# Kernel tuning notes

Measured on AMD Instinct MI355X. Metric: run time of the kernel, lower is better.

Reference implementation:

```python
import jax, jax.numpy as jnp
import numpy as np

C = 256


def _conv1x1(x, w, b):
    # x: [B,C,H,W], w: [O,C], b: [O] -> 1x1 conv == per-pixel linear
    return jnp.einsum('bchw,oc->bohw', x, w) + b[None, :, None, None]


def setup_inputs() -> dict:
    key = jax.random.key(0)
    ks = jax.random.split(key, 10)
    B, H, W = 4, 64, 64
    scale = 1.0 / np.sqrt(C)
    inp = {
        'F_c': jax.random.normal(ks[0], (B, C, H, W), jnp.float32),
        'F_s': jax.random.normal(ks[1], (B, C, H, W), jnp.float32),
        'w_f': jax.random.normal(ks[2], (C, C), jnp.float32) * scale,
        'b_f': jax.random.normal(ks[3], (C,), jnp.float32) * 0.01,
        'w_g': jax.random.normal(ks[4], (C, C), jnp.float32) * scale,
        'b_g': jax.random.normal(ks[5], (C,), jnp.float32) * 0.01,
        'w_h': jax.random.normal(ks[6], (C, C), jnp.float32) * scale,
        'b_h': jax.random.normal(ks[7], (C,), jnp.float32) * 0.01,
        'w_o': jax.random.normal(ks[8], (C, C), jnp.float32) * scale,
        'b_o': jax.random.normal(ks[9], (C,), jnp.float32) * 0.01,
    }
    return inp


def reference(F_c, F_s, w_f, b_f, w_g, b_g, w_h, b_h, w_o, b_o):
    b, c, h, w = F_c.shape
    Fq = _conv1x1(F_c, w_f, b_f).reshape(b, c, -1)   # [B,C,Nq]
    G = _conv1x1(F_s, w_g, b_g).reshape(b, c, -1)    # [B,C,Nk]
    Hv = _conv1x1(F_s, w_h, b_h).reshape(b, c, -1)   # [B,C,Nk]
    # S[b,i,j] = sum_c Fq[b,c,i] * G[b,c,j]; softmax over keys j
    S = jax.nn.softmax(jnp.einsum('bci,bcj->bij', Fq, G), axis=-1)
    # result[b,c,i] = sum_j Hv[b,c,j] * S[b,i,j]
    res = jnp.einsum('bcj,bij->bci', Hv, S).reshape(b, c, h, w)
    return _conv1x1(res, w_o, b_o)
```

## Files before the change

kernel.cpp:

```cpp
#include <hip/hip_runtime.h>
#include <hip/hip_bf16.h>

typedef __attribute__((ext_vector_type(8))) short bf16x8;
typedef __attribute__((ext_vector_type(4))) float f32x4;
typedef __attribute__((ext_vector_type(8))) _Float16 f16x8;
typedef __attribute__((ext_vector_type(8))) unsigned short u16x8;
typedef __attribute__((ext_vector_type(4))) unsigned short u16x4;
typedef unsigned int uint32;
typedef unsigned short ushort;

#define MFMA16(a, b, c) __builtin_amdgcn_mfma_f32_16x16x32_bf16((a), (b), (c), 0, 0, 0)
#define MFMA16F(a, b, c) __builtin_amdgcn_mfma_f32_16x16x32_f16((a), (b), (c), 0, 0, 0)

__device__ __forceinline__ ushort f2bf(float f) {
    __hip_bfloat16 h = __float2bfloat16(f);
    return __builtin_bit_cast(ushort, h);
}
__device__ __forceinline__ float bf2f(ushort u) {
    uint32 v = ((uint32)u) << 16;
    return __builtin_bit_cast(float, v);
}
__device__ __forceinline__ void gld16(const ushort* g, ushort* l) {
    __builtin_amdgcn_global_load_lds(
        (const __attribute__((address_space(1))) unsigned int*)g,
        (__attribute__((address_space(3))) unsigned int*)l, 16, 0, 0);
}

__global__ __launch_bounds__(256) void transpose_split(
    const float* __restrict__ Fc, const float* __restrict__ Fs,
    ushort* __restrict__ XcH, ushort* __restrict__ XcL,
    ushort* __restrict__ XsH, ushort* __restrict__ XsL) {
    __shared__ float lds[64][65];
    const int z = blockIdx.z;
    const int b = z & 3;
    const float* src = (z < 4) ? Fc : Fs;
    ushort* dh = (z < 4) ? XcH : XsH;
    ushort* dl = (z < 4) ? XcL : XsL;
    src += (size_t)b * 256 * 4096;
    dh += (size_t)b * 4096 * 256;
    dl += (size_t)b * 4096 * 256;
    const int i0 = blockIdx.x * 64;
    const int c0 = blockIdx.y * 64;
    const int t = threadIdx.x;
    const int rq = t >> 4;
    const int q4 = (t & 15) * 4;
#pragma unroll
    for (int p = 0; p < 4; p++) {
        int r = rq + p * 16;
        float4 v = *(const float4*)(src + (size_t)(c0 + r) * 4096 + i0 + q4);
        lds[q4 + 0][r] = v.x;
        lds[q4 + 1][r] = v.y;
        lds[q4 + 2][r] = v.z;
        lds[q4 + 3][r] = v.w;
    }
    __syncthreads();
#pragma unroll
    for (int p = 0; p < 4; p++) {
        int i = rq + p * 16;
        u16x4 hv, lv;
#pragma unroll
        for (int e = 0; e < 4; e++) {
            float f = lds[i][q4 + e];
            ushort hb = f2bf(f);
            hv[e] = hb;
            lv[e] = f2bf(f - bf2f(hb));
        }
        *(u16x4*)(dh + (size_t)(i0 + i) * 256 + c0 + q4) = hv;
        *(u16x4*)(dl + (size_t)(i0 + i) * 256 + c0 + q4) = lv;
    }
}

__global__ __launch_bounds__(256) void convert_weights(
    const float* __restrict__ wf, const float* __restrict__ wg,
    const float* __restrict__ wh, const float* __restrict__ wo,
    ushort* __restrict__ wfh, ushort* __restrict__ wfl,
    ushort* __restrict__ wgh, ushort* __restrict__ wgl,
    ushort* __restrict__ whb, ushort* __restrict__ wob) {
    const int t = blockIdx.x * 256 + threadIdx.x;
    const float L2E = 1.4426950408889634f;
    float sf = wf[t] * L2E;
    ushort hf = f2bf(sf);
    wfh[t] = hf;
    wfl[t] = f2bf(sf - bf2f(hf));
    float sg = wg[t];
    ushort hg = f2bf(sg);
    wgh[t] = hg;
    wgl[t] = f2bf(sg - bf2f(hg));
    whb[t] = f2bf(wh[t]);
    wob[t] = f2bf(wo[t]);
}

__global__ __launch_bounds__(256) void proj_qk(
    const ushort* __restrict__ XcH, const ushort* __restrict__ XcL,
    const ushort* __restrict__ XsH, const ushort* __restrict__ XsL,
    const ushort* __restrict__ wfh, const ushort* __restrict__ wfl,
    const ushort* __restrict__ wgh, const ushort* __restrict__ wgl,
    const float* __restrict__ bf_, const float* __restrict__ bg_,
    _Float16* __restrict__ QF, _Float16* __restrict__ KF) {
    const int y = blockIdx.y;
    const int isK = y >> 2;
    const int b = y & 3;
    const size_t bNC = (size_t)b * 4096 * 256;
    const ushort* Ah = (isK ? XsH : XcH) + bNC;
    const ushort* Al = (isK ? XsL : XcL) + bNC;
    const ushort* Bh = isK ? wgh : wfh;
    const ushort* Bl = isK ? wgl : wfl;
    const float* bias = isK ? bg_ : bf_;
    const float bscale = isK ? 1.0f : 1.4426950408889634f;
    _Float16* Co = (isK ? KF : QF) + bNC;
    const int m0 = (blockIdx.x & 63) * 64, n0 = (blockIdx.x >> 6) * 64;
    const int l = threadIdx.x & 63, wv = threadIdx.x >> 6;
    const int g = l >> 4, l15 = l & 15;
    const int mrow = m0 + wv * 16 + l15;

    f32x4 acc[4] = {{0, 0, 0, 0}, {0, 0, 0, 0}, {0, 0, 0, 0}, {0, 0, 0, 0}};
#pragma unroll
    for (int kk = 0; kk < 8; kk++) {
        bf16x8 ah = *(const bf16x8*)(Ah + (size_t)mrow * 256 + kk * 32 + g * 8);
        bf16x8 al = *(const bf16x8*)(Al + (size_t)mrow * 256 + kk * 32 + g * 8);
#pragma unroll
        for (int nt = 0; nt < 4; nt++) {
            const size_t boff = (size_t)(n0 + nt * 16 + l15) * 256 + kk * 32 + g * 8;
            bf16x8 bh = *(const bf16x8*)(Bh + boff);
            bf16x8 bl = *(const bf16x8*)(Bl + boff);
            acc[nt] = MFMA16(ah, bh, acc[nt]);
            acc[nt] = MFMA16(ah, bl, acc[nt]);
            acc[nt] = MFMA16(al, bh, acc[nt]);
        }
    }
#pragma unroll
    for (int nt = 0; nt < 4; nt++) {
        float bn = bias[n0 + nt * 16 + l15] * bscale;
#pragma unroll
        for (int r = 0; r < 4; r++) {
            int mr = m0 + wv * 16 + g * 4 + r;
            Co[(size_t)mr * 256 + n0 + nt * 16 + l15] = (_Float16)(acc[nt][r] + bn);
        }
    }
}

__global__ __launch_bounds__(256) void proj_v(
    const ushort* __restrict__ XsH, const ushort* __restrict__ whb,
    const float* __restrict__ bh_, ushort* __restrict__ Vv) {
    const int b = blockIdx.y;
    const size_t bNC = (size_t)b * 4096 * 256;
    const ushort* A = whb;
    const ushort* Bp = XsH + bNC;
    ushort* Cp = Vv + bNC;
    const int m0 = (blockIdx.x & 3) * 64, n0 = (blockIdx.x >> 2) * 64;
    const int l = threadIdx.x & 63, wv = threadIdx.x >> 6;
    const int g = l >> 4, l15 = l & 15;
    const int mrow = m0 + wv * 16 + l15;

    f32x4 acc[4] = {{0, 0, 0, 0}, {0, 0, 0, 0}, {0, 0, 0, 0}, {0, 0, 0, 0}};
#pragma unroll
    for (int kk = 0; kk < 8; kk++) {
        bf16x8 af = *(const bf16x8*)(A + (size_t)mrow * 256 + kk * 32 + g * 8);
#pragma unroll
        for (int nt = 0; nt < 4; nt++) {
            bf16x8 bfr = *(const bf16x8*)(Bp + (size_t)(n0 + nt * 16 + l15) * 256 + kk * 32 + g * 8);
            acc[nt] = MFMA16(af, bfr, acc[nt]);
        }
    }
#pragma unroll
    for (int nt = 0; nt < 4; nt++) {
#pragma unroll
        for (int r = 0; r < 4; r++) {
            int mr = m0 + wv * 16 + g * 4 + r;
            Cp[(size_t)mr * 4096 + n0 + nt * 16 + l15] = f2bf(acc[nt][r] + bh_[mr]);
        }
    }
}

__global__ __launch_bounds__(512, 2) void attn_split(
    const _Float16* __restrict__ QF, const _Float16* __restrict__ KF,
    const ushort* __restrict__ Vv, _Float16* __restrict__ Opart,
    float2* __restrict__ ML) {
    __shared__ __align__(16) _Float16 Kf[2][32 * 256];
    __shared__ __align__(16) ushort Vt[2][256 * 40];

    const int h = blockIdx.x;
    const int grp = h & 7;
    const int itile = h >> 3;
    const int b = grp >> 1;
    const int s = grp & 1;

    const int tid = threadIdx.x;
    const int l = tid & 63, wv = tid >> 6;
    const int g = l >> 4, l15 = l & 15;
    const int iw = itile * 128 + wv * 16;
    const _Float16* Qb = QF + ((size_t)b * 4096 + iw) * 256;
    const _Float16* Kb = KF + (size_t)b * 4096 * 256;
    const ushort* Vb = Vv + (size_t)b * 4096 * 256;

    f16x8 qf[8];
#pragma unroll
    for (int kk = 0; kk < 8; kk++)
        qf[kk] = *(const f16x8*)(Qb + (size_t)l15 * 256 + kk * 32 + g * 8);

    const int vch = tid >> 1;
    const int vko = (tid & 1) * 16;
    const ushort* Vsrc = Vb + (size_t)vch * 4096;

    f32x4 acc[16];
#pragma unroll
    for (int ct = 0; ct < 16; ct++) acc[ct] = (f32x4){0, 0, 0, 0};
    float M = -INFINITY, Lsum = 0.0f;

    const int jbeg = s * 2048, jend = jbeg + 2048;

    auto stageK = [&](int buf, int jj) {
        const _Float16* ks = Kb + (size_t)jj * 256;
#pragma unroll
        for (int q = 0; q < 2; q++) {
            int issue = wv * 2 + q;
            int row = issue * 2 + (l >> 5);
            int scol = ((l & 31) ^ row) * 8;
            gld16((const ushort*)(ks + (size_t)row * 256 + scol),
                  (ushort*)&Kf[buf][issue * 512]);
        }
    };

    stageK(0, jbeg);
    {
        u16x8 va = *(const u16x8*)(Vsrc + jbeg + vko);
        u16x8 vb2 = *(const u16x8*)(Vsrc + jbeg + vko + 8);
        asm volatile("s_waitcnt vmcnt(0)" ::: "memory");
        *(u16x8*)&Vt[0][vch * 40 + vko] = va;
        *(u16x8*)&Vt[0][vch * 40 + vko + 8] = vb2;
    }
    __syncthreads();

    int cur = 0;
    for (int j0 = jbeg; j0 < jend; j0 += 32) {
        const bool pre = (j0 + 32) < jend;
        u16x8 va, vb2;
        if (pre) {
            stageK(cur ^ 1, j0 + 32);
            va = *(const u16x8*)(Vsrc + (j0 + 32) + vko);
            vb2 = *(const u16x8*)(Vsrc + (j0 + 32) + vko + 8);
        }
        f32x4 s0e = {0, 0, 0, 0}, s0o = {0, 0, 0, 0};
        f32x4 s1e = {0, 0, 0, 0}, s1o = {0, 0, 0, 0};
        const int r1 = l15 + 16;
#pragma unroll
        for (int kk = 0; kk < 8; kk += 2) {
            {
                int cs = kk * 4 + g;
                f16x8 k0 = *(const f16x8*)&Kf[cur][l15 * 256 + ((cs ^ l15) & 31) * 8];
                f16x8 k1 = *(const f16x8*)&Kf[cur][r1 * 256 + ((cs ^ r1) & 31) * 8];
                s0e = MFMA16F(k0, qf[kk], s0e);
                s1e = MFMA16F(k1, qf[kk], s1e);
            }
            {
                int cs = (kk + 1) * 4 + g;
                f16x8 k0 = *(const f16x8*)&Kf[cur][l15 * 256 + ((cs ^ l15) & 31) * 8];
                f16x8 k1 = *(const f16x8*)&Kf[cur][r1 * 256 + ((cs ^ r1) & 31) * 8];
                s0o = MFMA16F(k0, qf[kk + 1], s0o);
                s1o = MFMA16F(k1, qf[kk + 1], s1o);
            }
        }
        f32x4 s0 = s0e + s0o;
        f32x4 s1 = s1e + s1o;
        float tm = fmaxf(fmaxf(fmaxf(s0[0], s0[1]), fmaxf(s0[2], s0[3])),
                         fmaxf(fmaxf(s1[0], s1[1]), fmaxf(s1[2], s1[3])));
        tm = fmaxf(tm, __shfl_xor(tm, 16));
        tm = fmaxf(tm, __shfl_xor(tm, 32));
        if (__any(tm - M > 8.0f)) {
            float newM = fmaxf(M, tm);
            float alpha = exp2f(M - newM);
            Lsum *= alpha;
            float ar[4];
#pragma unroll
            for (int r = 0; r < 4; r++) ar[r] = __shfl(alpha, g * 4 + r);
#pragma unroll
            for (int ct = 0; ct < 16; ct++) {
#pragma unroll
                for (int r = 0; r < 4; r++) acc[ct][r] *= ar[r];
            }
            M = newM;
        }
        float p[8];
#pragma unroll
        for (int r = 0; r < 4; r++) {
            p[r] = exp2f(s0[r] - M);
            p[4 + r] = exp2f(s1[r] - M);
        }
        Lsum += p[0] + p[1] + p[2] + p[3] + p[4] + p[5] + p[6] + p[7];

        uint32 pk[4];
        pk[0] = (uint32)f2bf(p[0]) | ((uint32)f2bf(p[1]) << 16);
        pk[1] = (uint32)f2bf(p[2]) | ((uint32)f2bf(p[3]) << 16);
        pk[2] = (uint32)f2bf(p[4]) | ((uint32)f2bf(p[5]) << 16);
        pk[3] = (uint32)f2bf(p[6]) | ((uint32)f2bf(p[7]) << 16);
        const int ts = g >> 1;
        const int s1l = l15 + ((g & 1) << 5);
        uint32 w0a = __shfl(pk[0], s1l), w0b = __shfl(pk[2], s1l);
        uint32 w1a = __shfl(pk[1], s1l), w1b = __shfl(pk[3], s1l);
        uint32 w2a = __shfl(pk[0], s1l + 16), w2b = __shfl(pk[2], s1l + 16);
        uint32 w3a = __shfl(pk[1], s1l + 16), w3b = __shfl(pk[3], s1l + 16);
        union { uint32 u[4]; bf16x8 v; } pun;
        pun.u[0] = ts ? w0b : w0a;
        pun.u[1] = ts ? w1b : w1a;
        pun.u[2] = ts ? w2b : w2a;
        pun.u[3] = ts ? w3b : w3a;
        bf16x8 pf = pun.v;

#pragma unroll
        for (int ct = 0; ct < 16; ct++) {
            bf16x8 vf = *(const bf16x8*)&Vt[cur][(ct * 16 + l15) * 40 + g * 8];
            acc[ct] = MFMA16(pf, vf, acc[ct]);
        }
        if (pre) {
            asm volatile("s_waitcnt vmcnt(0)" ::: "memory");
            *(u16x8*)&Vt[cur ^ 1][vch * 40 + vko] = va;
            *(u16x8*)&Vt[cur ^ 1][vch * 40 + vko + 8] = vb2;
        }
        __syncthreads();
        cur ^= 1;
    }
    float Lt = Lsum + __shfl_xor(Lsum, 16);
    Lt += __shfl_xor(Lt, 32);
    float inv = 1.0f / Lt;
    float ivr[4];
#pragma unroll
    for (int r = 0; r < 4; r++) ivr[r] = __shfl(inv, g * 4 + r);
    const size_t sb = (size_t)(s * 4 + b);
    _Float16* Ob = Opart + (sb * 4096 + iw) * 256;
#pragma unroll
    for (int ct = 0; ct < 16; ct++) {
#pragma unroll
        for (int r = 0; r < 4; r++)
            Ob[(size_t)(g * 4 + r) * 256 + ct * 16 + l15] =
                (_Float16)(acc[ct][r] * ivr[r]);
    }
    if (g == 0) {
        float2 ml;
        ml.x = M;
        ml.y = Lt;
        ML[sb * 4096 + iw + l15] = ml;
    }
}

__global__ __launch_bounds__(256) void attn_combine(
    const _Float16* __restrict__ Opart, const float2* __restrict__ ML,
    ushort* __restrict__ Rt) {
    const int b = blockIdx.y;
    const int i = blockIdx.x * 8 + (threadIdx.x >> 5);
    const int c0 = (threadIdx.x & 31) * 8;
    float2 ml0 = ML[(size_t)(0 * 4 + b) * 4096 + i];
    float2 ml1 = ML[(size_t)(1 * 4 + b) * 4096 + i];
    float Mmax = fmaxf(ml0.x, ml1.x);
    float w0 = ml0.y * exp2f(ml0.x - Mmax);
    float w1 = ml1.y * exp2f(ml1.x - Mmax);
    float inv = 1.0f / (w0 + w1);
    w0 *= inv;
    w1 *= inv;
    f16x8 v0 = *(const f16x8*)(Opart + ((size_t)(0 * 4 + b) * 4096 + i) * 256 + c0);
    f16x8 v1 = *(const f16x8*)(Opart + ((size_t)(1 * 4 + b) * 4096 + i) * 256 + c0);
    u16x8 r;
#pragma unroll
    for (int e = 0; e < 8; e++) r[e] = f2bf(w0 * (float)v0[e] + w1 * (float)v1[e]);
    *(u16x8*)(Rt + ((size_t)b * 4096 + i) * 256 + c0) = r;
}

__global__ __launch_bounds__(256) void out_proj(
    const ushort* __restrict__ wob, const ushort* __restrict__ Rt,
    const float* __restrict__ bo, float* __restrict__ Out) {
    const int b = blockIdx.y;
    const int m0 = (blockIdx.x & 3) * 64;
    const int n0 = (blockIdx.x >> 2) * 64;
    const int l = threadIdx.x & 63, wv = threadIdx.x >> 6;
    const int g = l >> 4, l15 = l & 15;
    const ushort* Bp = Rt + (size_t)b * 4096 * 256;
    float* Ob = Out + (size_t)b * 256 * 4096;
    const int mrow = m0 + wv * 16 + l15;

    f32x4 acc[4] = {{0, 0, 0, 0}, {0, 0, 0, 0}, {0, 0, 0, 0}, {0, 0, 0, 0}};
#pragma unroll
    for (int kk = 0; kk < 8; kk++) {
        bf16x8 af = *(const bf16x8*)(wob + (size_t)mrow * 256 + kk * 32 + g * 8);
#pragma unroll
        for (int nt = 0; nt < 4; nt++) {
            bf16x8 bfr = *(const bf16x8*)(Bp + (size_t)(n0 + nt * 16 + l15) * 256 + kk * 32 + g * 8);
            acc[nt] = MFMA16(af, bfr, acc[nt]);
        }
    }
#pragma unroll
    for (int nt = 0; nt < 4; nt++) {
#pragma unroll
        for (int r = 0; r < 4; r++) {
            int mr = m0 + wv * 16 + g * 4 + r;
            Ob[(size_t)mr * 4096 + n0 + nt * 16 + l15] = acc[nt][r] + bo[mr];
        }
    }
}

extern "C" void kernel_launch(void* const* d_in, const int* in_sizes, int n_in,
                              void* d_out, int out_size, void* d_ws, size_t ws_size,
                              hipStream_t stream) {
    const float* Fc = (const float*)d_in[0];
    const float* Fs = (const float*)d_in[1];
    const float* wf = (const float*)d_in[2];
    const float* bf_ = (const float*)d_in[3];
    const float* wg = (const float*)d_in[4];
    const float* bg = (const float*)d_in[5];
    const float* wh = (const float*)d_in[6];
    const float* bh = (const float*)d_in[7];
    const float* wo = (const float*)d_in[8];
    const float* bo = (const float*)d_in[9];
    float* Out = (float*)d_out;

    char* ws = (char*)d_ws;
    const size_t SZ = (size_t)4 * 4096 * 256 * 2;
    _Float16* QFp = (_Float16*)(ws + 0 * SZ);
    _Float16* KFp = (_Float16*)(ws + 1 * SZ);
    ushort* Vv  = (ushort*)(ws + 2 * SZ);
    ushort* XcH = (ushort*)(ws + 3 * SZ);
    ushort* XcL = (ushort*)(ws + 4 * SZ);
    ushort* XsH = (ushort*)(ws + 5 * SZ);
    ushort* XsL = (ushort*)(ws + 6 * SZ);
    _Float16* Opart = (_Float16*)(ws + 3 * SZ);
    char* wsw = ws + 7 * SZ;
    ushort* wfh = (ushort*)(wsw + 0 * 131072);
    ushort* wfl = (ushort*)(wsw + 1 * 131072);
    ushort* wgh = (ushort*)(wsw + 2 * 131072);
    ushort* wgl = (ushort*)(wsw + 3 * 131072);
    ushort* whb = (ushort*)(wsw + 4 * 131072);
    ushort* wob = (ushort*)(wsw + 5 * 131072);
    float2* ML = (float2*)(wsw + 6 * 131072);
    ushort* Rt = (ushort*)QFp;

    transpose_split<<<dim3(64, 4, 8), 256, 0, stream>>>(Fc, Fs, XcH, XcL, XsH, XsL);
    convert_weights<<<dim3(256), 256, 0, stream>>>(wf, wg, wh, wo, wfh, wfl, wgh, wgl, whb, wob);
    proj_qk<<<dim3(256, 8), 256, 0, stream>>>(XcH, XcL, XsH, XsL, wfh, wfl, wgh, wgl,
                                              bf_, bg, QFp, KFp);
    proj_v<<<dim3(256, 4), 256, 0, stream>>>(XsH, whb, bh, Vv);
    attn_split<<<dim3(256), 512, 0, stream>>>(QFp, KFp, Vv, Opart, ML);
    attn_combine<<<dim3(512, 4), 256, 0, stream>>>(Opart, ML, Rt);
    out_proj<<<dim3(256, 4), 256, 0, stream>>>(wob, Rt, bo, Out);
}
```

Before: 352.9 us.

## Switch pipeline to fp16, use 32x32 MFMA attention with 4-way key split

Activations are now converted to a single fp16 copy instead of bf16 hi/lo pairs. This halves transpose output traffic and drops one of the three MFMAs in the Q/K projection. The attention kernel moves to 32x32x16 f16 MFMA with 32 query rows per wave, uses v_permlane32_swap to repack P, and splits keys four ways instead of two, so the combine kernel now merges four partials. The intent is less memory traffic and better MFMA efficiency. The risks are fp16 range and precision limits on activations, plus extra partial-output traffic.

```diff
diff --git a/kernel.cpp b/kernel.cpp
--- a/kernel.cpp
+++ b/kernel.cpp
@@ -1,44 +1,37 @@
 #include <hip/hip_runtime.h>
 #include <hip/hip_bf16.h>
 
-typedef __attribute__((ext_vector_type(8))) short bf16x8;
 typedef __attribute__((ext_vector_type(4))) float f32x4;
+typedef __attribute__((ext_vector_type(16))) float f32x16;
 typedef __attribute__((ext_vector_type(8))) _Float16 f16x8;
-typedef __attribute__((ext_vector_type(8))) unsigned short u16x8;
-typedef __attribute__((ext_vector_type(4))) unsigned short u16x4;
+typedef __attribute__((ext_vector_type(4))) _Float16 f16x4;
 typedef unsigned int uint32;
 typedef unsigned short ushort;
 
-#define MFMA16(a, b, c) __builtin_amdgcn_mfma_f32_16x16x32_bf16((a), (b), (c), 0, 0, 0)
 #define MFMA16F(a, b, c) __builtin_amdgcn_mfma_f32_16x16x32_f16((a), (b), (c), 0, 0, 0)
-
-__device__ __forceinline__ ushort f2bf(float f) {
-    __hip_bfloat16 h = __float2bfloat16(f);
-    return __builtin_bit_cast(ushort, h);
-}
-__device__ __forceinline__ float bf2f(ushort u) {
-    uint32 v = ((uint32)u) << 16;
-    return __builtin_bit_cast(float, v);
-}
-__device__ __forceinline__ void gld16(const ushort* g, ushort* l) {
+#define MFMA32F(a, b, c) __builtin_amdgcn_mfma_f32_32x32x16_f16((a), (b), (c), 0, 0, 0)
+
+__device__ __forceinline__ uint32 pkf16(float a, float b) {
+    ushort ua = __builtin_bit_cast(ushort, (_Float16)a);
+    ushort ub = __builtin_bit_cast(ushort, (_Float16)b);
+    return (uint32)ua | ((uint32)ub << 16);
+}
+__device__ __forceinline__ void gld16(const _Float16* g, _Float16* l) {
     __builtin_amdgcn_global_load_lds(
         (const __attribute__((address_space(1))) unsigned int*)g,
         (__attribute__((address_space(3))) unsigned int*)l, 16, 0, 0);
 }
 
-__global__ __launch_bounds__(256) void transpose_split(
+__global__ __launch_bounds__(256) void transpose_f16(
     const float* __restrict__ Fc, const float* __restrict__ Fs,
-    ushort* __restrict__ XcH, ushort* __restrict__ XcL,
-    ushort* __restrict__ XsH, ushort* __restrict__ XsL) {
+    _Float16* __restrict__ Xc, _Float16* __restrict__ Xs) {
     __shared__ float lds[64][65];
     const int z = blockIdx.z;
     const int b = z & 3;
     const float* src = (z < 4) ? Fc : Fs;
-    ushort* dh = (z < 4) ? XcH : XsH;
-    ushort* dl = (z < 4) ? XcL : XsL;
+    _Float16* dst = (z < 4) ? Xc : Xs;
     src += (size_t)b * 256 * 4096;
-    dh += (size_t)b * 4096 * 256;
-    dl += (size_t)b * 4096 * 256;
+    dst += (size_t)b * 4096 * 256;
     const int i0 = blockIdx.x * 64;
     const int c0 = blockIdx.y * 64;
     const int t = threadIdx.x;
@@ -57,54 +50,46 @@
 #pragma unroll
     for (int p = 0; p < 4; p++) {
         int i = rq + p * 16;
-        u16x4 hv, lv;
-#pragma unroll
-        for (int e = 0; e < 4; e++) {
-            float f = lds[i][q4 + e];
-            ushort hb = f2bf(f);
-            hv[e] = hb;
-            lv[e] = f2bf(f - bf2f(hb));
-        }
-        *(u16x4*)(dh + (size_t)(i0 + i) * 256 + c0 + q4) = hv;
-        *(u16x4*)(dl + (size_t)(i0 + i) * 256 + c0 + q4) = lv;
+        f16x4 hv;
+#pragma unroll
+        for (int e = 0; e < 4; e++) hv[e] = (_Float16)lds[i][q4 + e];
+        *(f16x4*)(dst + (size_t)(i0 + i) * 256 + c0 + q4) = hv;
     }
 }
 
 __global__ __launch_bounds__(256) void convert_weights(
     const float* __restrict__ wf, const float* __restrict__ wg,
     const float* __restrict__ wh, const float* __restrict__ wo,
-    ushort* __restrict__ wfh, ushort* __restrict__ wfl,
-    ushort* __restrict__ wgh, ushort* __restrict__ wgl,
-    ushort* __restrict__ whb, ushort* __restrict__ wob) {
+    _Float16* __restrict__ wfh, _Float16* __restrict__ wfl,
+    _Float16* __restrict__ wgh, _Float16* __restrict__ wgl,
+    _Float16* __restrict__ whb, _Float16* __restrict__ wob) {
     const int t = blockIdx.x * 256 + threadIdx.x;
     const float L2E = 1.4426950408889634f;
     float sf = wf[t] * L2E;
-    ushort hf = f2bf(sf);
+    _Float16 hf = (_Float16)sf;
     wfh[t] = hf;
-    wfl[t] = f2bf(sf - bf2f(hf));
+    wfl[t] = (_Float16)(sf - (float)hf);
     float sg = wg[t];
-    ushort hg = f2bf(sg);
+    _Float16 hg = (_Float16)sg;
     wgh[t] = hg;
-    wgl[t] = f2bf(sg - bf2f(hg));
-    whb[t] = f2bf(wh[t]);
-    wob[t] = f2bf(wo[t]);
+    wgl[t] = (_Float16)(sg - (float)hg);
+    whb[t] = (_Float16)wh[t];
+    wob[t] = (_Float16)wo[t];
 }
 
 __global__ __launch_bounds__(256) void proj_qk(
-    const ushort* __restrict__ XcH, const ushort* __restrict__ XcL,
-    const ushort* __restrict__ XsH, const ushort* __restrict__ XsL,
-    const ushort* __restrict__ wfh, const ushort* __restrict__ wfl,
-    const ushort* __restrict__ wgh, const ushort* __restrict__ wgl,
+    const _Float16* __restrict__ Xc, const _Float16* __restrict__ Xs,
+    const _Float16* __restrict__ wfh, const _Float16* __restrict__ wfl,
+    const _Float16* __restrict__ wgh, const _Float16* __restrict__ wgl,
     const float* __restrict__ bf_, const float* __restrict__ bg_,
     _Float16* __restrict__ QF, _Float16* __restrict__ KF) {
     const int y = blockIdx.y;
     const int isK = y >> 2;
     const int b = y & 3;
     const size_t bNC = (size_t)b * 4096 * 256;
-    const ushort* Ah = (isK ? XsH : XcH) + bNC;
-    const ushort* Al = (isK ? XsL : XcL) + bNC;
-    const ushort* Bh = isK ? wgh : wfh;
-    const ushort* Bl = isK ? wgl : wfl;
+    const _Float16* A = (isK ? Xs : Xc) + bNC;
+    const _Float16* Bh = isK ? wgh : wfh;
+    const _Float16* Bl = isK ? wgl : wfl;
     const float* bias = isK ? bg_ : bf_;
     const float bscale = isK ? 1.0f : 1.4426950408889634f;
     _Float16* Co = (isK ? KF : QF) + bNC;
@@ -116,16 +101,14 @@
     f32x4 acc[4] = {{0, 0, 0, 0}, {0, 0, 0, 0}, {0, 0, 0, 0}, {0, 0, 0, 0}};
 #pragma unroll
     for (int kk = 0; kk < 8; kk++) {
-        bf16x8 ah = *(const bf16x8*)(Ah + (size_t)mrow * 256 + kk * 32 + g * 8);
-        bf16x8 al = *(const bf16x8*)(Al + (size_t)mrow * 256 + kk * 32 + g * 8);
+        f16x8 a = *(const f16x8*)(A + (size_t)mrow * 256 + kk * 32 + g * 8);
 #pragma unroll
         for (int nt = 0; nt < 4; nt++) {
             const size_t boff = (size_t)(n0 + nt * 16 + l15) * 256 + kk * 32 + g * 8;
-            bf16x8 bh = *(const bf16x8*)(Bh + boff);
-            bf16x8 bl = *(const bf16x8*)(Bl + boff);
-            acc[nt] = MFMA16(ah, bh, acc[nt]);
-            acc[nt] = MFMA16(ah, bl, acc[nt]);
-            acc[nt] = MFMA16(al, bh, acc[nt]);
+            f16x8 bh = *(const f16x8*)(Bh + boff);
+            f16x8 bl = *(const f16x8*)(Bl + boff);
+            acc[nt] = MFMA16F(a, bh, acc[nt]);
+            acc[nt] = MFMA16F(a, bl, acc[nt]);
         }
     }
 #pragma unroll
@@ -140,13 +123,12 @@
 }
 
 __global__ __launch_bounds__(256) void proj_v(
-    const ushort* __restrict__ XsH, const ushort* __restrict__ whb,
-    const float* __restrict__ bh_, ushort* __restrict__ Vv) {
+    const _Float16* __restrict__ Xs, const _Float16* __restrict__ whb,
+    const float* __restrict__ bh_, _Float16* __restrict__ VF) {
     const int b = blockIdx.y;
     const size_t bNC = (size_t)b * 4096 * 256;
-    const ushort* A = whb;
-    const ushort* Bp = XsH + bNC;
-    ushort* Cp = Vv + bNC;
+    const _Float16* Bp = Xs + bNC;
+    _Float16* Cp = VF + bNC;
     const int m0 = (blockIdx.x & 3) * 64, n0 = (blockIdx.x >> 2) * 64;
     const int l = threadIdx.x & 63, wv = threadIdx.x >> 6;
     const int g = l >> 4, l15 = l & 15;
@@ -155,11 +137,11 @@
     f32x4 acc[4] = {{0, 0, 0, 0}, {0, 0, 0, 0}, {0, 0, 0, 0}, {0, 0, 0, 0}};
 #pragma unroll
     for (int kk = 0; kk < 8; kk++) {
-        bf16x8 af = *(const bf16x8*)(A + (size_t)mrow * 256 + kk * 32 + g * 8);
+        f16x8 a = *(const f16x8*)(whb + (size_t)mrow * 256 + kk * 32 + g * 8);
 #pragma unroll
         for (int nt = 0; nt < 4; nt++) {
-            bf16x8 bfr = *(const bf16x8*)(Bp + (size_t)(n0 + nt * 16 + l15) * 256 + kk * 32 + g * 8);
-            acc[nt] = MFMA16(af, bfr, acc[nt]);
+            f16x8 bfr = *(const f16x8*)(Bp + (size_t)(n0 + nt * 16 + l15) * 256 + kk * 32 + g * 8);
+            acc[nt] = MFMA16F(a, bfr, acc[nt]);
         }
     }
 #pragma unroll
@@ -167,47 +149,47 @@
 #pragma unroll
         for (int r = 0; r < 4; r++) {
             int mr = m0 + wv * 16 + g * 4 + r;
-            Cp[(size_t)mr * 4096 + n0 + nt * 16 + l15] = f2bf(acc[nt][r] + bh_[mr]);
+            Cp[(size_t)mr * 4096 + n0 + nt * 16 + l15] = (_Float16)(acc[nt][r] + bh_[mr]);
         }
     }
 }
 
 __global__ __launch_bounds__(512, 2) void attn_split(
     const _Float16* __restrict__ QF, const _Float16* __restrict__ KF,
-    const ushort* __restrict__ Vv, _Float16* __restrict__ Opart,
+    const _Float16* __restrict__ VF, _Float16* __restrict__ Opart,
     float2* __restrict__ ML) {
-    __shared__ __align__(16) _Float16 Kf[2][32 * 256];
-    __shared__ __align__(16) ushort Vt[2][256 * 40];
+    __shared__ __align__(16) _Float16 Klds[2][32 * 256];
+    __shared__ __align__(16) _Float16 Vt[2][256 * 40];
 
     const int h = blockIdx.x;
-    const int grp = h & 7;
-    const int itile = h >> 3;
-    const int b = grp >> 1;
-    const int s = grp & 1;
+    const int grp = (h & 7) + 8 * ((h >> 3) & 1);
+    const int itile = h >> 4;
+    const int b = grp & 3, s = grp >> 2;
 
     const int tid = threadIdx.x;
     const int l = tid & 63, wv = tid >> 6;
-    const int g = l >> 4, l15 = l & 15;
-    const int iw = itile * 128 + wv * 16;
-    const _Float16* Qb = QF + ((size_t)b * 4096 + iw) * 256;
+    const int i31 = l & 31, hi = l >> 5;
+    const int iwq = itile * 256 + wv * 32;
+    const _Float16* Qb = QF + ((size_t)b * 4096 + iwq) * 256;
     const _Float16* Kb = KF + (size_t)b * 4096 * 256;
-    const ushort* Vb = Vv + (size_t)b * 4096 * 256;
-
-    f16x8 qf[8];
-#pragma unroll
-    for (int kk = 0; kk < 8; kk++)
-        qf[kk] = *(const f16x8*)(Qb + (size_t)l15 * 256 + kk * 32 + g * 8);
-
-    const int vch = tid >> 1;
-    const int vko = (tid & 1) * 16;
-    const ushort* Vsrc = Vb + (size_t)vch * 4096;
-
-    f32x4 acc[16];
-#pragma unroll
-    for (int ct = 0; ct < 16; ct++) acc[ct] = (f32x4){0, 0, 0, 0};
+    const _Float16* Vb = VF + (size_t)b * 4096 * 256;
+
+    f16x8 qf[16];
+#pragma unroll
+    for (int t = 0; t < 16; t++)
+        qf[t] = *(const f16x8*)(Qb + (size_t)i31 * 256 + t * 16 + hi * 8);
+
+    f32x16 acc[8];
+#pragma unroll
+    for (int ct = 0; ct < 8; ct++)
+#pragma unroll
+        for (int r = 0; r < 16; r++) acc[ct][r] = 0.0f;
     float M = -INFINITY, Lsum = 0.0f;
 
-    const int jbeg = s * 2048, jend = jbeg + 2048;
+    const int vch = tid >> 1, vko = (tid & 1) * 16;
+    const _Float16* Vsrc = Vb + (size_t)vch * 4096;
+
+    const int jbeg = s * 1024, jend = jbeg + 1024;
 
     auto stageK = [&](int buf, int jj) {
         const _Float16* ks = Kb + (size_t)jj * 256;
@@ -215,175 +197,174 @@
         for (int q = 0; q < 2; q++) {
             int issue = wv * 2 + q;
             int row = issue * 2 + (l >> 5);
-            int scol = ((l & 31) ^ row) * 8;
-            gld16((const ushort*)(ks + (size_t)row * 256 + scol),
-                  (ushort*)&Kf[buf][issue * 512]);
+            int scol = ((l & 31) ^ (row & 7)) * 8;
+            gld16(ks + (size_t)row * 256 + scol, &Klds[buf][issue * 512]);
         }
     };
 
     stageK(0, jbeg);
     {
-        u16x8 va = *(const u16x8*)(Vsrc + jbeg + vko);
-        u16x8 vb2 = *(const u16x8*)(Vsrc + jbeg + vko + 8);
+        f16x8 va = *(const f16x8*)(Vsrc + jbeg + vko);
+        f16x8 vb2 = *(const f16x8*)(Vsrc + jbeg + vko + 8);
         asm volatile("s_waitcnt vmcnt(0)" ::: "memory");
-        *(u16x8*)&Vt[0][vch * 40 + vko] = va;
-        *(u16x8*)&Vt[0][vch * 40 + vko + 8] = vb2;
+        *(f16x8*)&Vt[0][vch * 40 + vko] = va;
+        *(f16x8*)&Vt[0][vch * 40 + vko + 8] = vb2;
     }
     __syncthreads();
 
     int cur = 0;
     for (int j0 = jbeg; j0 < jend; j0 += 32) {
         const bool pre = (j0 + 32) < jend;
-        u16x8 va, vb2;
+        f16x8 va, vb2;
         if (pre) {
             stageK(cur ^ 1, j0 + 32);
-            va = *(const u16x8*)(Vsrc + (j0 + 32) + vko);
-            vb2 = *(const u16x8*)(Vsrc + (j0 + 32) + vko + 8);
-        }
-        f32x4 s0e = {0, 0, 0, 0}, s0o = {0, 0, 0, 0};
-        f32x4 s1e = {0, 0, 0, 0}, s1o = {0, 0, 0, 0};
-        const int r1 = l15 + 16;
-#pragma unroll
-        for (int kk = 0; kk < 8; kk += 2) {
-            {
-                int cs = kk * 4 + g;
-                f16x8 k0 = *(const f16x8*)&Kf[cur][l15 * 256 + ((cs ^ l15) & 31) * 8];
-                f16x8 k1 = *(const f16x8*)&Kf[cur][r1 * 256 + ((cs ^ r1) & 31) * 8];
-                s0e = MFMA16F(k0, qf[kk], s0e);
-                s1e = MFMA16F(k1, qf[kk], s1e);
-            }
-            {
-                int cs = (kk + 1) * 4 + g;
-                f16x8 k0 = *(const f16x8*)&Kf[cur][l15 * 256 + ((cs ^ l15) & 31) * 8];
-                f16x8 k1 = *(const f16x8*)&Kf[cur][r1 * 256 + ((cs ^ r1) & 31) * 8];
-                s0o = MFMA16F(k0, qf[kk + 1], s0o);
-                s1o = MFMA16F(k1, qf[kk + 1], s1o);
-            }
-        }
-        f32x4 s0 = s0e + s0o;
-        f32x4 s1 = s1e + s1o;
-        float tm = fmaxf(fmaxf(fmaxf(s0[0], s0[1]), fmaxf(s0[2], s0[3])),
-                         fmaxf(fmaxf(s1[0], s1[1]), fmaxf(s1[2], s1[3])));
-        tm = fmaxf(tm, __shfl_xor(tm, 16));
+            va = *(const f16x8*)(Vsrc + (j0 + 32) + vko);
+            vb2 = *(const f16x8*)(Vsrc + (j0 + 32) + vko + 8);
+        }
+        f32x16 sacc;
+#pragma unroll
+        for (int r = 0; r < 16; r++) sacc[r] = 0.0f;
+#pragma unroll
+        for (int t = 0; t < 16; t++) {
+            int pc = (2 * t + hi) ^ (i31 & 7);
+            f16x8 kf = *(const f16x8*)&Klds[cur][i31 * 256 + pc * 8];
+            sacc = MFMA32F(kf, qf[t], sacc);
+        }
+        float tm = sacc[0];
+#pragma unroll
+        for (int r = 1; r < 16; r++) tm = fmaxf(tm, sacc[r]);
         tm = fmaxf(tm, __shfl_xor(tm, 32));
         if (__any(tm - M > 8.0f)) {
             float newM = fmaxf(M, tm);
             float alpha = exp2f(M - newM);
             Lsum *= alpha;
-            float ar[4];
-#pragma unroll
-            for (int r = 0; r < 4; r++) ar[r] = __shfl(alpha, g * 4 + r);
-#pragma unroll
-            for (int ct = 0; ct < 16; ct++) {
-#pragma unroll
-                for (int r = 0; r < 4; r++) acc[ct][r] *= ar[r];
+            float ar[16];
+#pragma unroll
+            for (int r = 0; r < 16; r++)
+                ar[r] = __shfl(alpha, (r & 3) + 8 * (r >> 2) + 4 * hi);
+#pragma unroll
+            for (int ct = 0; ct < 8; ct++)
+#pragma unroll
+                for (int r = 0; r < 16; r++) acc[ct][r] *= ar[r];
+            M = newM;
+        }
+        float p[16], ps = 0.0f;
+#pragma unroll
+        for (int r = 0; r < 16; r++) {
+            p[r] = exp2f(sacc[r] - M);
+            ps += p[r];
+        }
+        Lsum += ps;
+        uint32 Pq[4][2];
+#pragma unroll
+        for (int q = 0; q < 4; q++) {
+            Pq[q][0] = pkf16(p[4 * q + 0], p[4 * q + 1]);
+            Pq[q][1] = pkf16(p[4 * q + 2], p[4 * q + 3]);
+        }
+#pragma unroll
+        for (int tp = 0; tp < 2; tp++) {
+            uint32 x0 = Pq[2 * tp][0], y0 = Pq[2 * tp + 1][0];
+            uint32 x1 = Pq[2 * tp][1], y1 = Pq[2 * tp + 1][1];
+            asm volatile("v_permlane32_swap_b32 %0, %1" : "+v"(x0), "+v"(y0));
+            asm volatile("v_permlane32_swap_b32 %0, %1" : "+v"(x1), "+v"(y1));
+            union { uint32 u[4]; f16x8 v; } pa;
+            pa.u[0] = x0;
+            pa.u[1] = x1;
+            pa.u[2] = y0;
+            pa.u[3] = y1;
+#pragma unroll
+            for (int ct = 0; ct < 8; ct++) {
+                f16x8 vf = *(const f16x8*)&Vt[cur][(ct * 32 + i31) * 40 + tp * 16 + hi * 8];
+                acc[ct] = MFMA32F(pa.v, vf, acc[ct]);
             }
-            M = newM;
-        }
-        float p[8];
-#pragma unroll
-        for (int r = 0; r < 4; r++) {
-            p[r] = exp2f(s0[r] - M);
-            p[4 + r] = exp2f(s1[r] - M);
-        }
-        Lsum += p[0] + p[1] + p[2] + p[3] + p[4] + p[5] + p[6] + p[7];
-
-        uint32 pk[4];
-        pk[0] = (uint32)f2bf(p[0]) | ((uint32)f2bf(p[1]) << 16);
-        pk[1] = (uint32)f2bf(p[2]) | ((uint32)f2bf(p[3]) << 16);
-        pk[2] = (uint32)f2bf(p[4]) | ((uint32)f2bf(p[5]) << 16);
-        pk[3] = (uint32)f2bf(p[6]) | ((uint32)f2bf(p[7]) << 16);
-        const int ts = g >> 1;
-        const int s1l = l15 + ((g & 1) << 5);
-        uint32 w0a = __shfl(pk[0], s1l), w0b = __shfl(pk[2], s1l);
-        uint32 w1a = __shfl(pk[1], s1l), w1b = __shfl(pk[3], s1l);
-        uint32 w2a = __shfl(pk[0], s1l + 16), w2b = __shfl(pk[2], s1l + 16);
-        uint32 w3a = __shfl(pk[1], s1l + 16), w3b = __shfl(pk[3], s1l + 16);
-        union { uint32 u[4]; bf16x8 v; } pun;
-        pun.u[0] = ts ? w0b : w0a;
-        pun.u[1] = ts ? w1b : w1a;
-        pun.u[2] = ts ? w2b : w2a;
-        pun.u[3] = ts ? w3b : w3a;
-        bf16x8 pf = pun.v;
-
-#pragma unroll
-        for (int ct = 0; ct < 16; ct++) {
-            bf16x8 vf = *(const bf16x8*)&Vt[cur][(ct * 16 + l15) * 40 + g * 8];
-            acc[ct] = MFMA16(pf, vf, acc[ct]);
         }
         if (pre) {
             asm volatile("s_waitcnt vmcnt(0)" ::: "memory");
-            *(u16x8*)&Vt[cur ^ 1][vch * 40 + vko] = va;
-            *(u16x8*)&Vt[cur ^ 1][vch * 40 + vko + 8] = vb2;
+            *(f16x8*)&Vt[cur ^ 1][vch * 40 + vko] = va;
+            *(f16x8*)&Vt[cur ^ 1][vch * 40 + vko + 8] = vb2;
         }
         __syncthreads();
         cur ^= 1;
     }
-    float Lt = Lsum + __shfl_xor(Lsum, 16);
-    Lt += __shfl_xor(Lt, 32);
+    float Lt = Lsum + __shfl_xor(Lsum, 32);
     float inv = 1.0f / Lt;
-    float ivr[4];
-#pragma unroll
-    for (int r = 0; r < 4; r++) ivr[r] = __shfl(inv, g * 4 + r);
+    float ivr[16];
+#pragma unroll
+    for (int r = 0; r < 16; r++)
+        ivr[r] = __shfl(inv, (r & 3) + 8 * (r >> 2) + 4 * hi);
     const size_t sb = (size_t)(s * 4 + b);
-    _Float16* Ob = Opart + (sb * 4096 + iw) * 256;
-#pragma unroll
-    for (int ct = 0; ct < 16; ct++) {
-#pragma unroll
-        for (int r = 0; r < 4; r++)
-            Ob[(size_t)(g * 4 + r) * 256 + ct * 16 + l15] =
-                (_Float16)(acc[ct][r] * ivr[r]);
-    }
-    if (g == 0) {
+    _Float16* Ob = Opart + (sb * 4096 + iwq) * 256;
+#pragma unroll
+    for (int ct = 0; ct < 8; ct++) {
+#pragma unroll
+        for (int r = 0; r < 16; r++) {
+            int ir = (r & 3) + 8 * (r >> 2) + 4 * hi;
+            Ob[(size_t)ir * 256 + ct * 32 + i31] = (_Float16)(acc[ct][r] * ivr[r]);
+        }
+    }
+    if (l < 32) {
         float2 ml;
         ml.x = M;
         ml.y = Lt;
-        ML[sb * 4096 + iw + l15] = ml;
+        ML[sb * 4096 + iwq + l] = ml;
     }
 }
 
 __global__ __launch_bounds__(256) void attn_combine(
     const _Float16* __restrict__ Opart, const float2* __restrict__ ML,
-    ushort* __restrict__ Rt) {
+    _Float16* __restrict__ Rt) {
     const int b = blockIdx.y;
     const int i = blockIdx.x * 8 + (threadIdx.x >> 5);
     const int c0 = (threadIdx.x & 31) * 8;
-    float2 ml0 = ML[(size_t)(0 * 4 + b) * 4096 + i];
-    float2 ml1 = ML[(size_t)(1 * 4 + b) * 4096 + i];
-    float Mmax = fmaxf(ml0.x, ml1.x);
-    float w0 = ml0.y * exp2f(ml0.x - Mmax);
-    float w1 = ml1.y * exp2f(ml1.x - Mmax);
-    float inv = 1.0f / (w0 + w1);
-    w0 *= inv;
-    w1 *= inv;
-    f16x8 v0 = *(const f16x8*)(Opart + ((size_t)(0 * 4 + b) * 4096 + i) * 256 + c0);
-    f16x8 v1 = *(const f16x8*)(Opart + ((size_t)(1 * 4 + b) * 4096 + i) * 256 + c0);
-    u16x8 r;
-#pragma unroll
-    for (int e = 0; e < 8; e++) r[e] = f2bf(w0 * (float)v0[e] + w1 * (float)v1[e]);
-    *(u16x8*)(Rt + ((size_t)b * 4096 + i) * 256 + c0) = r;
+    float m[4], lv[4];
+#pragma unroll
+    for (int s = 0; s < 4; s++) {
+        float2 ml = ML[(size_t)(s * 4 + b) * 4096 + i];
+        m[s] = ml.x;
+        lv[s] = ml.y;
+    }
+    float Mmax = fmaxf(fmaxf(m[0], m[1]), fmaxf(m[2], m[3]));
+    float w[4], denom = 0.0f;
+#pragma unroll
+    for (int s = 0; s < 4; s++) {
+        w[s] = lv[s] * exp2f(m[s] - Mmax);
+        denom += w[s];
+    }
+    float inv = 1.0f / denom;
+    float o[8] = {0, 0, 0, 0, 0, 0, 0, 0};
+#pragma unroll
+    for (int s = 0; s < 4; s++) {
+        float ws = w[s] * inv;
+        f16x8 v = *(const f16x8*)(Opart + ((size_t)(s * 4 + b) * 4096 + i) * 256 + c0);
+#pragma unroll
+        for (int e = 0; e < 8; e++) o[e] += ws * (float)v[e];
+    }
+    f16x8 r;
+#pragma unroll
+    for (int e = 0; e < 8; e++) r[e] = (_Float16)o[e];
+    *(f16x8*)(Rt + ((size_t)b * 4096 + i) * 256 + c0) = r;
 }
 
 __global__ __launch_bounds__(256) void out_proj(
-    const ushort* __restrict__ wob, const ushort* __restrict__ Rt,
+    const _Float16* __restrict__ wob, const _Float16* __restrict__ Rt,
     const float* __restrict__ bo, float* __restrict__ Out) {
     const int b = blockIdx.y;
     const int m0 = (blockIdx.x & 3) * 64;
     const int n0 = (blockIdx.x >> 2) * 64;
     const int l = threadIdx.x & 63, wv = threadIdx.x >> 6;
     const int g = l >> 4, l15 = l & 15;
-    const ushort* Bp = Rt + (size_t)b * 4096 * 256;
+    const _Float16* Bp = Rt + (size_t)b * 4096 * 256;
     float* Ob = Out + (size_t)b * 256 * 4096;
     const int mrow = m0 + wv * 16 + l15;
 
     f32x4 acc[4] = {{0, 0, 0, 0}, {0, 0, 0, 0}, {0, 0, 0, 0}, {0, 0, 0, 0}};
 #pragma unroll
     for (int kk = 0; kk < 8; kk++) {
-        bf16x8 af = *(const bf16x8*)(wob + (size_t)mrow * 256 + kk * 32 + g * 8);
+        f16x8 a = *(const f16x8*)(wob + (size_t)mrow * 256 + kk * 32 + g * 8);
 #pragma unroll
         for (int nt = 0; nt < 4; nt++) {
-            bf16x8 bfr = *(const bf16x8*)(Bp + (size_t)(n0 + nt * 16 + l15) * 256 + kk * 32 + g * 8);
-            acc[nt] = MFMA16(af, bfr, acc[nt]);
+            f16x8 bfr = *(const f16x8*)(Bp + (size_t)(n0 + nt * 16 + l15) * 256 + kk * 32 + g * 8);
+            acc[nt] = MFMA16F(a, bfr, acc[nt]);
         }
     }
 #pragma unroll
@@ -415,28 +396,25 @@
     const size_t SZ = (size_t)4 * 4096 * 256 * 2;
     _Float16* QFp = (_Float16*)(ws + 0 * SZ);
     _Float16* KFp = (_Float16*)(ws + 1 * SZ);
-    ushort* Vv  = (ushort*)(ws + 2 * SZ);
-    ushort* XcH = (ushort*)(ws + 3 * SZ);
-    ushort* XcL = (ushort*)(ws + 4 * SZ);
-    ushort* XsH = (ushort*)(ws + 5 * SZ);
-    ushort* XsL = (ushort*)(ws + 6 * SZ);
-    _Float16* Opart = (_Float16*)(ws + 3 * SZ);
-    char* wsw = ws + 7 * SZ;
-    ushort* wfh = (ushort*)(wsw + 0 * 131072);
-    ushort* wfl = (ushort*)(wsw + 1 * 131072);
-    ushort* wgh = (ushort*)(wsw + 2 * 131072);
-    ushort* wgl = (ushort*)(wsw + 3 * 131072);
-    ushort* whb = (ushort*)(wsw + 4 * 131072);
-    ushort* wob = (ushort*)(wsw + 5 * 131072);
+    _Float16* VFp = (_Float16*)(ws + 2 * SZ);
+    _Float16* Xc  = (_Float16*)(ws + 3 * SZ);
+    _Float16* Xs  = (_Float16*)(ws + 4 * SZ);
+    _Float16* Opart = (_Float16*)(ws + 5 * SZ);
+    char* wsw = ws + 9 * SZ;
+    _Float16* wfh = (_Float16*)(wsw + 0 * 131072);
+    _Float16* wfl = (_Float16*)(wsw + 1 * 131072);
+    _Float16* wgh = (_Float16*)(wsw + 2 * 131072);
+    _Float16* wgl = (_Float16*)(wsw + 3 * 131072);
+    _Float16* whb = (_Float16*)(wsw + 4 * 131072);
+    _Float16* wob = (_Float16*)(wsw + 5 * 131072);
     float2* ML = (float2*)(wsw + 6 * 131072);
-    ushort* Rt = (ushort*)QFp;
-
-    transpose_split<<<dim3(64, 4, 8), 256, 0, stream>>>(Fc, Fs, XcH, XcL, XsH, XsL);
+    _Float16* Rt = QFp;
+
+    transpose_f16<<<dim3(64, 4, 8), 256, 0, stream>>>(Fc, Fs, Xc, Xs);
     convert_weights<<<dim3(256), 256, 0, stream>>>(wf, wg, wh, wo, wfh, wfl, wgh, wgl, whb, wob);
-    proj_qk<<<dim3(256, 8), 256, 0, stream>>>(XcH, XcL, XsH, XsL, wfh, wfl, wgh, wgl,
-                                              bf_, bg, QFp, KFp);
-    proj_v<<<dim3(256, 4), 256, 0, stream>>>(XsH, whb, bh, Vv);
-    attn_split<<<dim3(256), 512, 0, stream>>>(QFp, KFp, Vv, Opart, ML);
+    proj_qk<<<dim3(256, 8), 256, 0, stream>>>(Xc, Xs, wfh, wfl, wgh, wgl, bf_, bg, QFp, KFp);
+    proj_v<<<dim3(256, 4), 256, 0, stream>>>(Xs, whb, bh, VFp);
+    attn_split<<<dim3(256), 512, 0, stream>>>(QFp, KFp, VFp, Opart, ML);
     attn_combine<<<dim3(512, 4), 256, 0, stream>>>(Opart, ML, Rt);
     out_proj<<<dim3(256, 4), 256, 0, stream>>>(wob, Rt, bo, Out);
 }
```

Measured after the change: 332.9 us. -5.7%, faster.
